# Kernel optimization log

Measured on AMD Instinct MI355X. Metric: run time of the kernel, lower is better.

Reference implementation:

```python
import jax, jax.numpy as jnp
import numpy as np

B, T = 256, 32
CNN_DIM, HW = 512, 14
HID, V = 8, 37


def setup_inputs() -> dict:
    key = jax.random.key(0)
    ks = jax.random.split(key, 10)
    s = 0.1  # param init scale
    return {
        "features": jax.random.normal(ks[0], (B, CNN_DIM, HW, HW), jnp.float32),
        "captions": jax.random.uniform(ks[1], (B, T, V), jnp.float32),
        "W_ih": jax.random.normal(ks[2], (4 * HID, V), jnp.float32) * s,
        "b_ih": jax.random.normal(ks[3], (4 * HID,), jnp.float32) * s,
        "W_hh": jax.random.normal(ks[4], (4 * HID, HID), jnp.float32) * s,
        "b_hh": jax.random.normal(ks[5], (4 * HID,), jnp.float32) * s,
        "W_in": jax.random.normal(ks[6], (V, CNN_DIM), jnp.float32) * s,
        "b_in": jax.random.normal(ks[7], (V,), jnp.float32) * s,
        "W_out": jax.random.normal(ks[8], (V, HID), jnp.float32) * s,
        "b_out": jax.random.normal(ks[9], (V,), jnp.float32) * s,
        "isTraining": 1,
    }


def _lstm_step(h, c, x, W_ih, b_ih, W_hh, b_hh):
    # PyTorch LSTMCell gate order: i, f, g, o
    gates = x @ W_ih.T + b_ih + h @ W_hh.T + b_hh  # [B, 4*HID]
    i, f, g, o = jnp.split(gates, 4, axis=1)
    c = jax.nn.sigmoid(f) * c + jax.nn.sigmoid(i) * jnp.tanh(g)
    h = jax.nn.sigmoid(o) * jnp.tanh(c)
    return h, c


def reference(features, captions, W_ih, b_ih, W_hh, b_hh, W_in, b_in, W_out, b_out, isTraining):
    bsz, seq_len, vocab = captions.shape
    hid = W_hh.shape[1]
    # AdaptiveAvgPool2d(1) + flatten + fc_in
    pooled = features.mean(axis=(2, 3))          # [B, cnn_dim]
    x0 = pooled @ W_in.T + b_in                  # [B, V]
    h0 = jnp.zeros((bsz, hid), features.dtype)
    c0 = jnp.zeros((bsz, hid), features.dtype)

    if isTraining:
        # teacher forcing: inputs are [x0, captions[:,0], ..., captions[:,T-2]]
        xs = jnp.concatenate([x0[:, None, :], captions[:, : seq_len - 1, :]], axis=1)

        def step(carry, x):
            h, c = carry
            h, c = _lstm_step(h, c, x, W_ih, b_ih, W_hh, b_hh)
            out = h @ W_out.T + b_out
            return (h, c), out

        _, outs = jax.lax.scan(step, (h0, c0), jnp.swapaxes(xs, 0, 1))
        outputs = jnp.swapaxes(outs, 0, 1)       # [B, T, V]
    else:
        # greedy feedback: feed previous (pre-softmax) fc_out logits
        h, c = _lstm_step(h0, c0, x0, W_ih, b_ih, W_hh, b_hh)
        out0 = h @ W_out.T + b_out

        def step(carry, _):
            h, c, prev = carry
            h, c = _lstm_step(h, c, prev, W_ih, b_ih, W_hh, b_hh)
            out = h @ W_out.T + b_out
            return (h, c, out), out

        _, outs = jax.lax.scan(step, (h, c, out0), None, length=seq_len - 1)
        outputs = jnp.concatenate([out0[:, None, :], jnp.swapaxes(outs, 0, 1)], axis=1)

    # Faithful to original: Softmax(dim=1) is over the TIME axis
    return jax.nn.softmax(outputs, axis=1)
```

## Files before the change

### kernel.cpp

```cpp
#include <hip/hip_runtime.h>
#include <math.h>


#define BDIM 512

__device__ __forceinline__ float wave_reduce_sum(float v) {
#pragma unroll
    for (int off = 32; off; off >>= 1) v += __shfl_down(v, off, 64);
    return v;
}

__device__ __forceinline__ float sigf(float x) { return 1.0f / (1.0f + __expf(-x)); }
__device__ __forceinline__ float tanhfast(float x) { return 1.0f - 2.0f / (__expf(2.0f * x) + 1.0f); }

__global__ __launch_bounds__(BDIM) void lstm_fused(
    const float* __restrict__ features, const float* __restrict__ captions,
    const float* __restrict__ W_ih, const float* __restrict__ b_ih,
    const float* __restrict__ W_hh, const float* __restrict__ b_hh,
    const float* __restrict__ W_in, const float* __restrict__ b_in,
    const float* __restrict__ W_out, const float* __restrict__ b_out,
    const int* __restrict__ isTraining, float* __restrict__ out)
{
    constexpr int T = 32, V = 37, HID = 8, C = 512, NPIX = 196, G = 32;

    __shared__ float pooled[C];
    __shared__ float xs[T * V];
    __shared__ float wih[G * V];
    __shared__ float xg[T * G];
    __shared__ float hist[T * HID];
    __shared__ float lg[T * V];
    __shared__ float bsum[G];
    __shared__ float inv_s[V];

    const int b    = blockIdx.x;
    const int tid  = threadIdx.x;
    const int lane = tid & 63;
    const int w    = tid >> 6;

    const float* featB = features + (size_t)b * C * NPIX;
    const int li = (lane < 49) ? lane : 0;
    for (int grp = 0; grp < 8; ++grp) {
        float s[8];
#pragma unroll
        for (int u = 0; u < 8; ++u) {
            const int c = w + 8 * (grp * 8 + u);
            const float4 v = ((const float4*)(featB + c * NPIX))[li];
            const float s4 = (v.x + v.y) + (v.z + v.w);
            s[u] = (lane < 49) ? s4 : 0.0f;
        }
#pragma unroll
        for (int u = 0; u < 8; ++u) {
            const float tot = wave_reduce_sum(s[u]);
            if (lane == 0) pooled[w + 8 * (grp * 8 + u)] = tot * (1.0f / 196.0f);
        }
    }

    for (int i = tid; i < G * V; i += BDIM) wih[i] = W_ih[i];
    for (int i = tid + V; i < T * V; i += BDIM) xs[i] = captions[(size_t)b * T * V + (i - V)];
    if (tid < G) bsum[tid] = b_ih[tid] + b_hh[tid];
    __syncthreads();

    for (int v = w; v < V; v += 8) {
        const float* wr = W_in + (size_t)v * C;
        float p = 0.0f;
#pragma unroll
        for (int k = 0; k < 8; ++k) p += pooled[lane + 64 * k] * wr[lane + 64 * k];
        p = wave_reduce_sum(p);
        if (lane == 0) xs[v] = p + b_in[v];
    }
    __syncthreads();

    for (int e = tid; e < T * G; e += BDIM) {
        const int t = e >> 5, j = e & 31;
        const float* xr = xs + t * V;
        const float* wr = wih + j * V;
        float acc = bsum[j];
#pragma unroll
        for (int v = 0; v < V; ++v) acc += xr[v] * wr[v];
        xg[e] = acc;
    }
    __syncthreads();

    const bool train = (isTraining[0] != 0);
    if (w == 0) {
        const int j = lane & 31;
        const int k8 = lane & 7;
        float whh_r[HID];
#pragma unroll
        for (int k = 0; k < HID; ++k) whh_r[k] = W_hh[j * HID + k];
        float wout_r[HID];
        float bout_r = 0.0f;
        if (lane < V) {
#pragma unroll
            for (int k = 0; k < HID; ++k) wout_r[k] = W_out[lane * HID + k];
            bout_r = b_out[lane];
        }
        float h = 0.0f, c = 0.0f;
        float prevout = 0.0f;

        for (int t = 0; t < T; ++t) {
            float gate;
            if (train || t == 0) {
                gate = xg[t * G + j];
            } else {
                float acc = bsum[j];
                const float* wr = wih + j * V;
#pragma unroll
                for (int v = 0; v < V; ++v) acc += __shfl(prevout, v, 64) * wr[v];
                gate = acc;
            }
#pragma unroll
            for (int k = 0; k < HID; ++k) gate += __shfl(h, k, 64) * whh_r[k];

            const int sec = lane >> 3;
            const float a = (sec == 2) ? tanhfast(gate) : sigf(gate);

            const float ig = __shfl(a, k8, 64);
            const float fg = __shfl(a, 8 + k8, 64);
            const float gg = __shfl(a, 16 + k8, 64);
            const float og = __shfl(a, 24 + k8, 64);
            c = fg * c + ig * gg;
            h = og * tanhfast(c);

            if (train) {
                if (lane < HID) hist[t * HID + lane] = h;
            } else {
                float o = bout_r;
#pragma unroll
                for (int k = 0; k < HID; ++k) o += __shfl(h, k, 64) * wout_r[k];
                if (lane < V) lg[t * V + lane] = o;
                prevout = o;
            }
        }
    }
    __syncthreads();

    if (train) {
        for (int e = tid; e < T * V; e += BDIM) {
            const int t = e / V, v = e - t * V;
            const float* hr = hist + t * HID;
            const float* wr = W_out + v * HID;
            float acc = b_out[v];
#pragma unroll
            for (int k = 0; k < HID; ++k) acc += hr[k] * wr[k];
            lg[e] = acc;
        }
    }
    __syncthreads();

    if (tid < V) {
        float m = -1e30f;
#pragma unroll
        for (int t = 0; t < T; ++t) m = fmaxf(m, lg[t * V + tid]);
        float s = 0.0f;
#pragma unroll
        for (int t = 0; t < T; ++t) {
            const float e = __expf(lg[t * V + tid] - m);
            lg[t * V + tid] = e;
            s += e;
        }
        inv_s[tid] = 1.0f / s;
    }
    __syncthreads();

    float* outB = out + (size_t)b * T * V;
    for (int e = tid; e < T * V; e += BDIM) {
        const int t = e / V, v = e - t * V;
        outB[e] = lg[e] * inv_s[v];
    }
}

extern "C" void kernel_launch(void* const* d_in, const int* in_sizes, int n_in,
                              void* d_out, int out_size, void* d_ws, size_t ws_size,
                              hipStream_t stream) {
    const float* features = (const float*)d_in[0];
    const float* captions = (const float*)d_in[1];
    const float* W_ih     = (const float*)d_in[2];
    const float* b_ih     = (const float*)d_in[3];
    const float* W_hh     = (const float*)d_in[4];
    const float* b_hh     = (const float*)d_in[5];
    const float* W_in     = (const float*)d_in[6];
    const float* b_in     = (const float*)d_in[7];
    const float* W_out    = (const float*)d_in[8];
    const float* b_out    = (const float*)d_in[9];
    const int*   isTrain  = (const int*)d_in[10];
    float* out = (float*)d_out;

    lstm_fused<<<256, BDIM, 0, stream>>>(features, captions, W_ih, b_ih, W_hh, b_hh,
                                         W_in, b_in, W_out, b_out, isTrain, out);
}
```

Measured before the change: 182.2 us.

## Split feature pooling into separate wide-grid kernel with register prefetch

Moves the average-pooling over the 100MB feature tensor out of the fused per-batch kernel into its own kernel with 1024 blocks of 256 threads, each handling 128 channels, and double-buffers loads in registers. The pooled results go through the workspace to the remaining LSTM kernel, which now only loads 512 floats per batch. The aim is more memory-level parallelism and occupancy on the bandwidth-bound pooling phase. The cost is a second launch and a global round-trip for the pooled vector.

```diff
diff --git a/kernel.cpp b/kernel.cpp
--- a/kernel.cpp
+++ b/kernel.cpp
@@ -13,15 +13,53 @@
 __device__ __forceinline__ float sigf(float x) { return 1.0f / (1.0f + __expf(-x)); }
 __device__ __forceinline__ float tanhfast(float x) { return 1.0f - 2.0f / (__expf(2.0f * x) + 1.0f); }
 
-__global__ __launch_bounds__(BDIM) void lstm_fused(
-    const float* __restrict__ features, const float* __restrict__ captions,
+__global__ __launch_bounds__(256, 4) void pool_kernel(
+    const float* __restrict__ features, float* __restrict__ pooled )
+{
+    constexpr int NPIX = 196, C = 512;
+    const int b    = blockIdx.x >> 2;
+    const int q    = blockIdx.x & 3;
+    const int lane = threadIdx.x & 63;
+    const int w    = threadIdx.x >> 6;
+    const int c0   = q * 128 + w * 32;
+    const float* featB = features + (size_t)b * C * NPIX;
+    const int li = (lane < 49) ? lane : 0;
+
+    float4 buf[8];
+#pragma unroll
+    for (int u = 0; u < 8; ++u)
+        buf[u] = ((const float4*)(featB + (c0 + u) * NPIX))[li];
+
+    for (int grp = 0; grp < 4; ++grp) {
+        float s[8];
+#pragma unroll
+        for (int u = 0; u < 8; ++u) {
+            const float4 v = buf[u];
+            s[u] = (lane < 49) ? (v.x + v.y) + (v.z + v.w) : 0.0f;
+        }
+        if (grp < 3) {
+#pragma unroll
+            for (int u = 0; u < 8; ++u)
+                buf[u] = ((const float4*)(featB + (c0 + (grp + 1) * 8 + u) * NPIX))[li];
+        }
+#pragma unroll
+        for (int u = 0; u < 8; ++u) {
+            const float tot = wave_reduce_sum(s[u]);
+            if (lane == 0)
+                pooled[(size_t)b * C + c0 + grp * 8 + u] = tot * (1.0f / 196.0f);
+        }
+    }
+}
+
+__global__ __launch_bounds__(BDIM) void lstm_rest(
+    const float* __restrict__ pooled_g, const float* __restrict__ captions,
     const float* __restrict__ W_ih, const float* __restrict__ b_ih,
     const float* __restrict__ W_hh, const float* __restrict__ b_hh,
     const float* __restrict__ W_in, const float* __restrict__ b_in,
     const float* __restrict__ W_out, const float* __restrict__ b_out,
     const int* __restrict__ isTraining, float* __restrict__ out)
 {
-    constexpr int T = 32, V = 37, HID = 8, C = 512, NPIX = 196, G = 32;
+    constexpr int T = 32, V = 37, HID = 8, C = 512, G = 32;
 
     __shared__ float pooled[C];
     __shared__ float xs[T * V];
@@ -37,24 +75,7 @@
     const int lane = tid & 63;
     const int w    = tid >> 6;
 
-    const float* featB = features + (size_t)b * C * NPIX;
-    const int li = (lane < 49) ? lane : 0;
-    for (int grp = 0; grp < 8; ++grp) {
-        float s[8];
-#pragma unroll
-        for (int u = 0; u < 8; ++u) {
-            const int c = w + 8 * (grp * 8 + u);
-            const float4 v = ((const float4*)(featB + c * NPIX))[li];
-            const float s4 = (v.x + v.y) + (v.z + v.w);
-            s[u] = (lane < 49) ? s4 : 0.0f;
-        }
-#pragma unroll
-        for (int u = 0; u < 8; ++u) {
-            const float tot = wave_reduce_sum(s[u]);
-            if (lane == 0) pooled[w + 8 * (grp * 8 + u)] = tot * (1.0f / 196.0f);
-        }
-    }
-
+    pooled[tid] = pooled_g[(size_t)b * C + tid];
     for (int i = tid; i < G * V; i += BDIM) wih[i] = W_ih[i];
     for (int i = tid + V; i < T * V; i += BDIM) xs[i] = captions[(size_t)b * T * V + (i - V)];
     if (tid < G) bsum[tid] = b_ih[tid] + b_hh[tid];
@@ -186,6 +207,9 @@
     const int*   isTrain  = (const int*)d_in[10];
     float* out = (float*)d_out;
 
-    lstm_fused<<<256, BDIM, 0, stream>>>(features, captions, W_ih, b_ih, W_hh, b_hh,
-                                         W_in, b_in, W_out, b_out, isTrain, out);
-}
+    float* pooled = (float*)d_ws;
+
+    pool_kernel<<<256 * 4, 256, 0, stream>>>(features, pooled);
+    lstm_rest<<<256, BDIM, 0, stream>>>(pooled, captions, W_ih, b_ih, W_hh, b_hh,
+                                        W_in, b_in, W_out, b_out, isTrain, out);
+}
```

Result: slower. 189.7 us (+4.1%).

## Split global average pooling into a separate wide-grid kernel

Applied to the files above, without the earlier changes.

Moves the feature-map average pooling out of the per-batch fused kernel into its own kernel launched with 8192 blocks of 1024 threads, one wave per channel, writing pooled values to workspace. The LSTM kernel then loads the pooled vector from global memory. The aim is to spread the dominant ~100MB feature read across the whole GPU instead of 256 blocks, at the cost of an extra launch and a small workspace round trip.

```diff
diff --git a/kernel.cpp b/kernel.cpp
--- a/kernel.cpp
+++ b/kernel.cpp
@@ -13,15 +13,32 @@
 __device__ __forceinline__ float sigf(float x) { return 1.0f / (1.0f + __expf(-x)); }
 __device__ __forceinline__ float tanhfast(float x) { return 1.0f - 2.0f / (__expf(2.0f * x) + 1.0f); }
 
-__global__ __launch_bounds__(BDIM) void lstm_fused(
-    const float* __restrict__ features, const float* __restrict__ captions,
+__global__ void pool_kernel(
+    const float* __restrict__ features, float* __restrict__ pooled )
+{
+    constexpr int NPIX = 196;
+    const int wid  = (blockIdx.x << 4) + (threadIdx.x >> 6);
+    const int lane = threadIdx.x & 63;
+    const float* base = features + (size_t)wid * NPIX;
+
+    float s = 0.0f;
+    if (lane < 49) {
+        const float4 v = ((const float4*)base)[lane];
+        s = (v.x + v.y) + (v.z + v.w);
+    }
+    s = wave_reduce_sum(s);
+    if (lane == 0) pooled[wid] = s * (1.0f / 196.0f);
+}
+
+__global__ __launch_bounds__(BDIM) void lstm_rest(
+    const float* __restrict__ pooled_g, const float* __restrict__ captions,
     const float* __restrict__ W_ih, const float* __restrict__ b_ih,
     const float* __restrict__ W_hh, const float* __restrict__ b_hh,
     const float* __restrict__ W_in, const float* __restrict__ b_in,
     const float* __restrict__ W_out, const float* __restrict__ b_out,
     const int* __restrict__ isTraining, float* __restrict__ out)
 {
-    constexpr int T = 32, V = 37, HID = 8, C = 512, NPIX = 196, G = 32;
+    constexpr int T = 32, V = 37, HID = 8, C = 512, G = 32;
 
     __shared__ float pooled[C];
     __shared__ float xs[T * V];
@@ -37,24 +54,7 @@
     const int lane = tid & 63;
     const int w    = tid >> 6;
 
-    const float* featB = features + (size_t)b * C * NPIX;
-    const int li = (lane < 49) ? lane : 0;
-    for (int grp = 0; grp < 8; ++grp) {
-        float s[8];
-#pragma unroll
-        for (int u = 0; u < 8; ++u) {
-            const int c = w + 8 * (grp * 8 + u);
-            const float4 v = ((const float4*)(featB + c * NPIX))[li];
-            const float s4 = (v.x + v.y) + (v.z + v.w);
-            s[u] = (lane < 49) ? s4 : 0.0f;
-        }
-#pragma unroll
-        for (int u = 0; u < 8; ++u) {
-            const float tot = wave_reduce_sum(s[u]);
-            if (lane == 0) pooled[w + 8 * (grp * 8 + u)] = tot * (1.0f / 196.0f);
-        }
-    }
-
+    pooled[tid] = pooled_g[(size_t)b * C + tid];
     for (int i = tid; i < G * V; i += BDIM) wih[i] = W_ih[i];
     for (int i = tid + V; i < T * V; i += BDIM) xs[i] = captions[(size_t)b * T * V + (i - V)];
     if (tid < G) bsum[tid] = b_ih[tid] + b_hh[tid];
@@ -186,6 +186,9 @@
     const int*   isTrain  = (const int*)d_in[10];
     float* out = (float*)d_out;
 
-    lstm_fused<<<256, BDIM, 0, stream>>>(features, captions, W_ih, b_ih, W_hh, b_hh,
-                                         W_in, b_in, W_out, b_out, isTrain, out);
+    float* pooled = (float*)d_ws;
+
+    pool_kernel<<<8192, 1024, 0, stream>>>(features, pooled);
+    lstm_rest<<<256, BDIM, 0, stream>>>(pooled, captions, W_ih, b_ih, W_hh, b_hh,
+                                        W_in, b_in, W_out, b_out, isTrain, out);
 }
```

After: 185.2 us. About the same (+1.6%).
